# Kernel tuning notes

Measured on AMD Instinct MI355X. Metric: run time of the kernel, lower is better.

## Reference

```python
import jax, jax.numpy as jnp
import numpy as np

B, T, C = 4, 2048, 1024
N_HEAD = 16
HEAD_DIM = C // N_HEAD


def setup_inputs() -> dict:
    key = jax.random.key(0)
    k1, k2, k3 = jax.random.split(key, 3)
    x = jax.random.normal(k1, (B, T, C), dtype=jnp.float32)
    # Linear weights stored as (in, out); scaled like typical init
    w_qkv = jax.random.normal(k2, (C, 3 * C), dtype=jnp.float32) * (1.0 / np.sqrt(C))
    w_proj = jax.random.normal(k3, (C, C), dtype=jnp.float32) * (1.0 / np.sqrt(C))
    return {"x": x, "w_qkv": w_qkv, "w_proj": w_proj}


def reference(x, w_qkv, w_proj):
    b, t, c = x.shape
    qkv = x @ w_qkv                      # (B,T,3C)
    q, k, v = jnp.split(qkv, 3, axis=-1)
    # (B,H,T,D)
    def to_heads(a):
        return a.reshape(b, t, N_HEAD, HEAD_DIM).transpose(0, 2, 1, 3)
    q, k, v = to_heads(q), to_heads(k), to_heads(v)
    scale = 1.0 / np.sqrt(HEAD_DIM).astype(np.float32)
    att = jnp.einsum('bhqd,bhkd->bhqk', q, k) * scale   # (B,H,T,T)
    causal = jnp.tril(jnp.ones((t, t), dtype=bool))
    att = jnp.where(causal[None, None, :, :], att, -jnp.inf)
    att = jax.nn.softmax(att, axis=-1)
    # dropout p=0.0 (eval) -> identity
    y = jnp.einsum('bhqk,bhkd->bhqd', att, v)            # (B,H,T,D)
    y = y.transpose(0, 2, 1, 3).reshape(b, t, c)
    return y @ w_proj
```

## Files before the change

kernel.cpp:

```cpp
#include <hip/hip_runtime.h>
#include <hip/hip_bf16.h>
#include <stdint.h>

#define Bsz 4
#define Tsz 2048
#define Csz 1024
#define Hn  16
#define Dh  64
#define BH  (Bsz*Hn)
#define Mrows (Bsz*Tsz)
#define N1  (3*Csz)

typedef short s16x8 __attribute__((ext_vector_type(8)));
typedef short s16x4 __attribute__((ext_vector_type(4)));
typedef float fx4   __attribute__((ext_vector_type(4)));

static __device__ __forceinline__ short f2bf(float x) {
  __hip_bfloat16 h = __float2bfloat16(x);
  return __builtin_bit_cast(short, h);
}

#define GLDS16(g, l) __builtin_amdgcn_global_load_lds( \
    (const __attribute__((address_space(1))) void*)(g), \
    (__attribute__((address_space(3))) void*)(l), 16, 0, 0)

__global__ void cvt_kernel(const float* __restrict__ in, short* __restrict__ out, int n4) {
  int i = blockIdx.x * blockDim.x + threadIdx.x;
  int stride = blockDim.x * gridDim.x;
  for (; i < n4; i += stride) {
    float4 v = ((const float4*)in)[i];
    s16x4 o;
    o.x = f2bf(v.x); o.y = f2bf(v.y); o.z = f2bf(v.z); o.w = f2bf(v.w);
    ((s16x4*)out)[i] = o;
  }
}

__global__ void transpose_cvt_kernel(const float* __restrict__ w, short* __restrict__ wt,
                                     int K, int N) {
  __shared__ float tile[32][33];
  int tc = threadIdx.x & 31;
  int tr = threadIdx.x >> 5;
  int n0 = blockIdx.x * 32;
  int k0 = blockIdx.y * 32;
#pragma unroll
  for (int p = 0; p < 4; p++) {
    int r = tr + p*8;
    tile[r][tc] = w[(size_t)(k0 + r) * N + (n0 + tc)];
  }
  __syncthreads();
#pragma unroll
  for (int p = 0; p < 4; p++) {
    int r = tr + p*8;
    wt[(size_t)(n0 + r) * K + (k0 + tc)] = f2bf(tile[tc][r]);
  }
}

__global__ __launch_bounds__(256) void gemm_bt_kernel(
    const short* __restrict__ A, const short* __restrict__ Bt,
    float* __restrict__ Cf,
    short* __restrict__ Qo, short* __restrict__ Ko, short* __restrict__ Vo,
    int Mdim, int Ndim, int Kdim, int mode)
{
  __shared__ __align__(16) short sA[128*64];
  __shared__ __align__(16) short sB[128*64];
  const int tid  = threadIdx.x;
  const int lane = tid & 63;
  const int lr   = lane & 15;
  const int lq   = lane >> 4;
  const int wv   = tid >> 6;
  const int sw   = lr & 7;
  const int nb   = Ndim >> 7;
  const int bm   = (int)blockIdx.x / nb;
  const int bn   = (int)blockIdx.x % nb;
  const int m_off = (wv & 1) << 6;
  const int n_off = (wv >> 1) << 6;

  const short* Ab = A  + (size_t)bm * 128 * Kdim;
  const short* Bb = Bt + (size_t)bn * 128 * Kdim;

  fx4 acc[4][4];
#pragma unroll
  for (int i = 0; i < 4; i++)
#pragma unroll
    for (int j = 0; j < 4; j++) acc[i][j] = (fx4){0.f, 0.f, 0.f, 0.f};

  int cr[4], cg[4];
#pragma unroll
  for (int i = 0; i < 4; i++) {
    int c = tid + 256*i;
    cr[i] = c >> 3;
    cg[i] = ((c & 7) ^ (cr[i] & 7)) * 8;
  }

  for (int k0 = 0; k0 < Kdim; k0 += 64) {
    __syncthreads();
#pragma unroll
    for (int i = 0; i < 4; i++) {
      GLDS16(Ab + (size_t)cr[i] * Kdim + k0 + cg[i], sA + (tid + 256*i) * 8);
      GLDS16(Bb + (size_t)cr[i] * Kdim + k0 + cg[i], sB + (tid + 256*i) * 8);
    }
    __syncthreads();
    s16x8 af[4][2], bf[4][2];
#pragma unroll
    for (int mt = 0; mt < 4; mt++)
#pragma unroll
      for (int kk = 0; kk < 2; kk++)
        af[mt][kk] = *(const s16x8*)(sA + (m_off + mt*16 + lr)*64 + ((kk*4 + lq) ^ sw)*8);
#pragma unroll
    for (int nt = 0; nt < 4; nt++)
#pragma unroll
      for (int kk = 0; kk < 2; kk++)
        bf[nt][kk] = *(const s16x8*)(sB + (n_off + nt*16 + lr)*64 + ((kk*4 + lq) ^ sw)*8);
#pragma unroll
    for (int kk = 0; kk < 2; kk++)
#pragma unroll
      for (int mt = 0; mt < 4; mt++)
#pragma unroll
        for (int nt = 0; nt < 4; nt++)
          acc[mt][nt] = __builtin_amdgcn_mfma_f32_16x16x32_bf16(af[mt][kk], bf[nt][kk], acc[mt][nt], 0, 0, 0);
  }

  const int gm0 = bm*128 + m_off;
  const int gn0 = bn*128 + n_off;
  if (mode == 0) {
#pragma unroll
    for (int mt = 0; mt < 4; mt++)
#pragma unroll
      for (int nt = 0; nt < 4; nt++) {
        int col = gn0 + nt*16 + lr;
#pragma unroll
        for (int r = 0; r < 4; r++) {
          int row = gm0 + mt*16 + lq*4 + r;
          Cf[(size_t)row * Ndim + col] = acc[mt][nt][r];
        }
      }
  } else {
#pragma unroll
    for (int mt = 0; mt < 4; mt++)
#pragma unroll
      for (int nt = 0; nt < 4; nt++) {
        int n   = gn0 + nt*16 + lr;
        int sec = n >> 10;
        int cc  = n & 1023;
        int hh  = cc >> 6;
        int dd  = cc & 63;
#pragma unroll
        for (int r = 0; r < 4; r++) {
          int m  = gm0 + mt*16 + lq*4 + r;
          int bb = m >> 11;
          int tt = m & 2047;
          int bh = bb * Hn + hh;
          short v = f2bf(acc[mt][nt][r]);
          if (sec == 0)      Qo[((size_t)bh * Tsz + tt) * Dh + dd] = v;
          else if (sec == 1) Ko[((size_t)bh * Tsz + tt) * Dh + dd] = v;
          else               Vo[((size_t)bh * Dh + dd) * Tsz + tt] = v;
        }
      }
  }
}

#define PPITCH 72

__global__ __launch_bounds__(256) void attn_kernel(
    const short* __restrict__ Qb, const short* __restrict__ Kb,
    const short* __restrict__ Vt, short* __restrict__ Y)
{
  __shared__ __align__(16) short sK[64*64];
  __shared__ __align__(16) short sV[64*64];
  __shared__ __align__(16) short pbuf[4][32*PPITCH];
  const int tid  = threadIdx.x;
  const int lane = tid & 63;
  const int wv   = tid >> 6;
  const int lr   = lane & 15;
  const int lq   = lane >> 4;
  const int sw   = lr & 7;
  const int bh   = blockIdx.x;
  const int qb   = 15 - (int)blockIdx.y;
  const int b    = bh >> 4;
  const int h    = bh & 15;
  const int q0   = qb*128 + wv*32;

  const short* Qp = Qb + (size_t)bh * Tsz * Dh;
  const short* Kp = Kb + (size_t)bh * Tsz * Dh;
  const short* Vp = Vt + (size_t)bh * Dh * Tsz;
  short* pb = pbuf[wv];

  const int c0 = tid,       r0 = c0 >> 3, g0 = (((c0 & 7) ^ (r0 & 7)) * 8);
  const int c1 = tid + 256, r1 = c1 >> 3, g1 = (((c1 & 7) ^ (r1 & 7)) * 8);

  s16x8 bq[2][2];
#pragma unroll
  for (int j = 0; j < 2; j++)
#pragma unroll
    for (int kk = 0; kk < 2; kk++)
      bq[j][kk] = *(const s16x8*)(Qp + (size_t)(q0 + 16*j + lr)*Dh + kk*32 + lq*8);

  fx4 o[2][4];
#pragma unroll
  for (int j = 0; j < 2; j++)
#pragma unroll
    for (int i = 0; i < 4; i++) o[j][i] = (fx4){0.f, 0.f, 0.f, 0.f};
  float li[2] = {0.f, 0.f};
  const float sc = 0.125f * 1.44269504f;

  const int ntiles = 2*qb + 2;
  for (int kt = 0; kt < ntiles; kt++) {
    const int kbase = kt*64;
    __syncthreads();
    GLDS16(Kp + (size_t)(kbase + r0)*Dh + g0, sK + c0*8);
    GLDS16(Kp + (size_t)(kbase + r1)*Dh + g1, sK + c1*8);
    GLDS16(Vp + (size_t)r0*Tsz + kbase + g0, sV + c0*8);
    GLDS16(Vp + (size_t)r1*Tsz + kbase + g1, sV + c1*8);
    __syncthreads();

    if (kbase <= q0 + 31) {
      const bool masked = (kbase + 63 > q0);

      fx4 s[2][4];
#pragma unroll
      for (int j = 0; j < 2; j++)
#pragma unroll
        for (int mt = 0; mt < 4; mt++) s[j][mt] = (fx4){0.f,0.f,0.f,0.f};
#pragma unroll
      for (int mt = 0; mt < 4; mt++)
#pragma unroll
        for (int kk = 0; kk < 2; kk++) {
          const s16x8 akf = *(const s16x8*)(sK + (mt*16 + lr)*64 + ((kk*4 + lq) ^ sw)*8);
          s[0][mt] = __builtin_amdgcn_mfma_f32_16x16x32_bf16(akf, bq[0][kk], s[0][mt], 0, 0, 0);
          s[1][mt] = __builtin_amdgcn_mfma_f32_16x16x32_bf16(akf, bq[1][kk], s[1][mt], 0, 0, 0);
        }

#pragma unroll
      for (int j = 0; j < 2; j++) {
        const int qg = q0 + 16*j + lr;
        float p[16];
#pragma unroll
        for (int mt = 0; mt < 4; mt++)
#pragma unroll
          for (int r = 0; r < 4; r++) {
            float v = s[j][mt][r];
            if (masked) {
              int jg = kbase + mt*16 + lq*4 + r;
              v = (jg <= qg) ? v : -1e30f;
            }
            p[mt*4 + r] = __builtin_amdgcn_exp2f(v * sc);
          }
        float s8[8];
#pragma unroll
        for (int i = 0; i < 8; i++) s8[i] = p[i] + p[i+8];
        float s4[4];
#pragma unroll
        for (int i = 0; i < 4; i++) s4[i] = s8[i] + s8[i+4];
        li[j] += (s4[0] + s4[2]) + (s4[1] + s4[3]);
#pragma unroll
        for (int mt = 0; mt < 4; mt++) {
          s16x4 pk;
          pk.x = f2bf(p[mt*4+0]); pk.y = f2bf(p[mt*4+1]);
          pk.z = f2bf(p[mt*4+2]); pk.w = f2bf(p[mt*4+3]);
          *(s16x4*)(pb + (16*j + lr)*PPITCH + mt*16 + lq*4) = pk;
        }
      }
      __asm__ __volatile__("" ::: "memory");
      s16x8 pf[2][2];
#pragma unroll
      for (int j = 0; j < 2; j++)
#pragma unroll
        for (int kk = 0; kk < 2; kk++)
          pf[j][kk] = *(const s16x8*)(pb + (16*j + lr)*PPITCH + kk*32 + lq*8);
      __asm__ __volatile__("" ::: "memory");

#pragma unroll
      for (int dt = 0; dt < 4; dt++)
#pragma unroll
        for (int kk = 0; kk < 2; kk++) {
          const s16x8 avf = *(const s16x8*)(sV + (dt*16 + lr)*64 + ((kk*4 + lq) ^ sw)*8);
          o[0][dt] = __builtin_amdgcn_mfma_f32_16x16x32_bf16(avf, pf[0][kk], o[0][dt], 0, 0, 0);
          o[1][dt] = __builtin_amdgcn_mfma_f32_16x16x32_bf16(avf, pf[1][kk], o[1][dt], 0, 0, 0);
        }
    }
  }

#pragma unroll
  for (int j = 0; j < 2; j++) {
    float l = li[j];
    l += __shfl_xor(l, 16);
    l += __shfl_xor(l, 32);
    float inv = 1.0f / l;
#pragma unroll
    for (int dt = 0; dt < 4; dt++) {
      s16x4 yk;
      yk.x = f2bf(o[j][dt][0]*inv); yk.y = f2bf(o[j][dt][1]*inv);
      yk.z = f2bf(o[j][dt][2]*inv); yk.w = f2bf(o[j][dt][3]*inv);
      *(s16x4*)(Y + ((size_t)b*Tsz + q0 + 16*j + lr)*Csz + h*Dh + dt*16 + lq*4) = yk;
    }
  }
}

extern "C" void kernel_launch(void* const* d_in, const int* in_sizes, int n_in,
                              void* d_out, int out_size, void* d_ws, size_t ws_size,
                              hipStream_t stream)
{
  const float* x  = (const float*)d_in[0];
  const float* wq = (const float*)d_in[1];
  const float* wp = (const float*)d_in[2];
  float* out = (float*)d_out;

  char* ws = (char*)d_ws;
  size_t off = 0;
  short* xb  = (short*)(ws + off); off += (size_t)Mrows*Csz*2;
  short* wqT = (short*)(ws + off); off += (size_t)N1*Csz*2;
  short* wpT = (short*)(ws + off); off += (size_t)Csz*Csz*2;
  short* Qb  = (short*)(ws + off); off += (size_t)BH*Tsz*Dh*2;
  short* Kb  = (short*)(ws + off); off += (size_t)BH*Tsz*Dh*2;
  short* Vt  = (short*)(ws + off); off += (size_t)BH*Dh*Tsz*2;
  short* Yb  = (short*)(ws + off); off += (size_t)Mrows*Csz*2;

  cvt_kernel<<<1024, 256, 0, stream>>>(x, xb, Mrows*Csz/4);
  transpose_cvt_kernel<<<dim3(N1/32, Csz/32), 256, 0, stream>>>(wq, wqT, Csz, N1);
  transpose_cvt_kernel<<<dim3(Csz/32, Csz/32), 256, 0, stream>>>(wp, wpT, Csz, Csz);
  gemm_bt_kernel<<<(Mrows/128)*(N1/128), 256, 0, stream>>>(
      xb, wqT, nullptr, Qb, Kb, Vt, Mrows, N1, Csz, 1);
  attn_kernel<<<dim3(BH, Tsz/128), 256, 0, stream>>>(Qb, Kb, Vt, Yb);
  gemm_bt_kernel<<<(Mrows/128)*(Csz/128), 256, 0, stream>>>(
      Yb, wpT, out, nullptr, nullptr, nullptr, Mrows, Csz, Csz, 0);
}
```

Measured before the change: 278.4 us.

## Double-buffer LDS in QKV GEMM and attention, vectorize transposed V store

```diff
diff --git a/kernel.cpp b/kernel.cpp
--- a/kernel.cpp
+++ b/kernel.cpp
@@ -55,20 +55,59 @@
   }
 }
 
+static __device__ __forceinline__ void gemm_stage(
+    const short* __restrict__ Ab, const short* __restrict__ Bb, int Kdim, int k0,
+    short* __restrict__ sA, short* __restrict__ sB, int tid)
+{
+#pragma unroll
+  for (int i = 0; i < 2; i++) {
+    int c  = tid + 256*i;
+    int mr = c >> 3;
+    int l  = (c & 7) ^ (mr & 7);
+    int row = mr*2 + (l >> 2);
+    int ko  = (l & 3) * 8;
+    GLDS16(Ab + (size_t)row * Kdim + k0 + ko, sA + c*8);
+    GLDS16(Bb + (size_t)row * Kdim + k0 + ko, sB + c*8);
+  }
+}
+
+static __device__ __forceinline__ void gemm_compute(
+    const short* __restrict__ sA, const short* __restrict__ sB,
+    int m_off, int n_off, int lr, int lq, fx4 acc[4][4])
+{
+  s16x8 af[4], bf[4];
+#pragma unroll
+  for (int mt = 0; mt < 4; mt++) {
+    int m = m_off + mt*16 + lr, mr = m >> 1;
+    int p = (((m & 1)*4 + lq)) ^ (mr & 7);
+    af[mt] = *(const s16x8*)(sA + mr*64 + p*8);
+  }
+#pragma unroll
+  for (int nt = 0; nt < 4; nt++) {
+    int n = n_off + nt*16 + lr, nr = n >> 1;
+    int p = (((n & 1)*4 + lq)) ^ (nr & 7);
+    bf[nt] = *(const s16x8*)(sB + nr*64 + p*8);
+  }
+#pragma unroll
+  for (int mt = 0; mt < 4; mt++)
+#pragma unroll
+    for (int nt = 0; nt < 4; nt++)
+      acc[mt][nt] = __builtin_amdgcn_mfma_f32_16x16x32_bf16(af[mt], bf[nt], acc[mt][nt], 0, 0, 0);
+}
+
 __global__ __launch_bounds__(256) void gemm_bt_kernel(
     const short* __restrict__ A, const short* __restrict__ Bt,
     float* __restrict__ Cf,
     short* __restrict__ Qo, short* __restrict__ Ko, short* __restrict__ Vo,
     int Mdim, int Ndim, int Kdim, int mode)
 {
-  __shared__ __align__(16) short sA[128*64];
-  __shared__ __align__(16) short sB[128*64];
+  __shared__ __align__(16) short sA[2][128*32];
+  __shared__ __align__(16) short sB[2][128*32];
   const int tid  = threadIdx.x;
   const int lane = tid & 63;
   const int lr   = lane & 15;
   const int lq   = lane >> 4;
   const int wv   = tid >> 6;
-  const int sw   = lr & 7;
   const int nb   = Ndim >> 7;
   const int bm   = (int)blockIdx.x / nb;
   const int bn   = (int)blockIdx.x % nb;
@@ -84,40 +123,15 @@
 #pragma unroll
     for (int j = 0; j < 4; j++) acc[i][j] = (fx4){0.f, 0.f, 0.f, 0.f};
 
-  int cr[4], cg[4];
-#pragma unroll
-  for (int i = 0; i < 4; i++) {
-    int c = tid + 256*i;
-    cr[i] = c >> 3;
-    cg[i] = ((c & 7) ^ (cr[i] & 7)) * 8;
-  }
-
-  for (int k0 = 0; k0 < Kdim; k0 += 64) {
+  const int NIT = Kdim >> 5;
+  gemm_stage(Ab, Bb, Kdim, 0, sA[0], sB[0], tid);
+  for (int it = 0; it < NIT; it += 2) {
     __syncthreads();
-#pragma unroll
-    for (int i = 0; i < 4; i++) {
-      GLDS16(Ab + (size_t)cr[i] * Kdim + k0 + cg[i], sA + (tid + 256*i) * 8);
-      GLDS16(Bb + (size_t)cr[i] * Kdim + k0 + cg[i], sB + (tid + 256*i) * 8);
-    }
+    if (it + 1 < NIT) gemm_stage(Ab, Bb, Kdim, (it+1)*32, sA[1], sB[1], tid);
+    gemm_compute(sA[0], sB[0], m_off, n_off, lr, lq, acc);
     __syncthreads();
-    s16x8 af[4][2], bf[4][2];
-#pragma unroll
-    for (int mt = 0; mt < 4; mt++)
-#pragma unroll
-      for (int kk = 0; kk < 2; kk++)
-        af[mt][kk] = *(const s16x8*)(sA + (m_off + mt*16 + lr)*64 + ((kk*4 + lq) ^ sw)*8);
-#pragma unroll
-    for (int nt = 0; nt < 4; nt++)
-#pragma unroll
-      for (int kk = 0; kk < 2; kk++)
-        bf[nt][kk] = *(const s16x8*)(sB + (n_off + nt*16 + lr)*64 + ((kk*4 + lq) ^ sw)*8);
-#pragma unroll
-    for (int kk = 0; kk < 2; kk++)
-#pragma unroll
-      for (int mt = 0; mt < 4; mt++)
-#pragma unroll
-        for (int nt = 0; nt < 4; nt++)
-          acc[mt][nt] = __builtin_amdgcn_mfma_f32_16x16x32_bf16(af[mt][kk], bf[nt][kk], acc[mt][nt], 0, 0, 0);
+    if (it + 2 < NIT) gemm_stage(Ab, Bb, Kdim, (it+2)*32, sA[0], sB[0], tid);
+    gemm_compute(sA[1], sB[1], m_off, n_off, lr, lq, acc);
   }
 
   const int gm0 = bm*128 + m_off;
@@ -144,29 +158,120 @@
         int cc  = n & 1023;
         int hh  = cc >> 6;
         int dd  = cc & 63;
-#pragma unroll
-        for (int r = 0; r < 4; r++) {
-          int m  = gm0 + mt*16 + lq*4 + r;
-          int bb = m >> 11;
-          int tt = m & 2047;
-          int bh = bb * Hn + hh;
-          short v = f2bf(acc[mt][nt][r]);
-          if (sec == 0)      Qo[((size_t)bh * Tsz + tt) * Dh + dd] = v;
-          else if (sec == 1) Ko[((size_t)bh * Tsz + tt) * Dh + dd] = v;
-          else               Vo[((size_t)bh * Dh + dd) * Tsz + tt] = v;
+        if (sec == 2) {
+          int tt0 = gm0 + mt*16 + lq*4;
+          int bb  = tt0 >> 11;
+          int bh  = bb * Hn + hh;
+          s16x4 pk;
+          pk.x = f2bf(acc[mt][nt][0]); pk.y = f2bf(acc[mt][nt][1]);
+          pk.z = f2bf(acc[mt][nt][2]); pk.w = f2bf(acc[mt][nt][3]);
+          *(s16x4*)(Vo + ((size_t)bh * Dh + dd) * Tsz + (tt0 & 2047)) = pk;
+        } else {
+#pragma unroll
+          for (int r = 0; r < 4; r++) {
+            int m  = gm0 + mt*16 + lq*4 + r;
+            int bb = m >> 11;
+            int tt = m & 2047;
+            int bh = bb * Hn + hh;
+            short v = f2bf(acc[mt][nt][r]);
+            if (sec == 0) Qo[((size_t)bh * Tsz + tt) * Dh + dd] = v;
+            else          Ko[((size_t)bh * Tsz + tt) * Dh + dd] = v;
+          }
         }
       }
   }
 }
 
 #define PPITCH 72
+
+static __device__ __forceinline__ void attn_stage(
+    const short* __restrict__ Kp, const short* __restrict__ Vp, int kbase,
+    short* __restrict__ sK, short* __restrict__ sV,
+    int c0, int r0, int g0, int c1, int r1, int g1)
+{
+  GLDS16(Kp + (size_t)(kbase + r0)*Dh + g0, sK + c0*8);
+  GLDS16(Kp + (size_t)(kbase + r1)*Dh + g1, sK + c1*8);
+  GLDS16(Vp + (size_t)r0*Tsz + kbase + g0, sV + c0*8);
+  GLDS16(Vp + (size_t)r1*Tsz + kbase + g1, sV + c1*8);
+}
+
+static __device__ __forceinline__ void attn_compute(
+    const short* __restrict__ sK, const short* __restrict__ sV,
+    int kbase, int q0, int lr, int lq, int sw,
+    short* __restrict__ pb, const s16x8 bq[2][2], fx4 o[2][4], float li[2])
+{
+  const float sc = 0.125f * 1.44269504f;
+  const bool masked = (kbase + 63 > q0);
+
+  fx4 s[2][4];
+#pragma unroll
+  for (int j = 0; j < 2; j++)
+#pragma unroll
+    for (int mt = 0; mt < 4; mt++) s[j][mt] = (fx4){0.f,0.f,0.f,0.f};
+#pragma unroll
+  for (int mt = 0; mt < 4; mt++)
+#pragma unroll
+    for (int kk = 0; kk < 2; kk++) {
+      const s16x8 akf = *(const s16x8*)(sK + (mt*16 + lr)*64 + ((kk*4 + lq) ^ sw)*8);
+      s[0][mt] = __builtin_amdgcn_mfma_f32_16x16x32_bf16(akf, bq[0][kk], s[0][mt], 0, 0, 0);
+      s[1][mt] = __builtin_amdgcn_mfma_f32_16x16x32_bf16(akf, bq[1][kk], s[1][mt], 0, 0, 0);
+    }
+
+#pragma unroll
+  for (int j = 0; j < 2; j++) {
+    const int qg = q0 + 16*j + lr;
+    float p[16];
+#pragma unroll
+    for (int mt = 0; mt < 4; mt++)
+#pragma unroll
+      for (int r = 0; r < 4; r++) {
+        float v = s[j][mt][r];
+        if (masked) {
+          int jg = kbase + mt*16 + lq*4 + r;
+          v = (jg <= qg) ? v : -1e30f;
+        }
+        p[mt*4 + r] = __builtin_amdgcn_exp2f(v * sc);
+      }
+    float s8[8];
+#pragma unroll
+    for (int i = 0; i < 8; i++) s8[i] = p[i] + p[i+8];
+    float s4[4];
+#pragma unroll
+    for (int i = 0; i < 4; i++) s4[i] = s8[i] + s8[i+4];
+    li[j] += (s4[0] + s4[2]) + (s4[1] + s4[3]);
+#pragma unroll
+    for (int mt = 0; mt < 4; mt++) {
+      s16x4 pk;
+      pk.x = f2bf(p[mt*4+0]); pk.y = f2bf(p[mt*4+1]);
+      pk.z = f2bf(p[mt*4+2]); pk.w = f2bf(p[mt*4+3]);
+      *(s16x4*)(pb + (16*j + lr)*PPITCH + mt*16 + lq*4) = pk;
+    }
+  }
+  __asm__ __volatile__("" ::: "memory");
+  s16x8 pf[2][2];
+#pragma unroll
+  for (int j = 0; j < 2; j++)
+#pragma unroll
+    for (int kk = 0; kk < 2; kk++)
+      pf[j][kk] = *(const s16x8*)(pb + (16*j + lr)*PPITCH + kk*32 + lq*8);
+  __asm__ __volatile__("" ::: "memory");
+
+#pragma unroll
+  for (int dt = 0; dt < 4; dt++)
+#pragma unroll
+    for (int kk = 0; kk < 2; kk++) {
+      const s16x8 avf = *(const s16x8*)(sV + (dt*16 + lr)*64 + ((kk*4 + lq) ^ sw)*8);
+      o[0][dt] = __builtin_amdgcn_mfma_f32_16x16x32_bf16(avf, pf[0][kk], o[0][dt], 0, 0, 0);
+      o[1][dt] = __builtin_amdgcn_mfma_f32_16x16x32_bf16(avf, pf[1][kk], o[1][dt], 0, 0, 0);
+    }
+}
 
 __global__ __launch_bounds__(256) void attn_kernel(
     const short* __restrict__ Qb, const short* __restrict__ Kb,
     const short* __restrict__ Vt, short* __restrict__ Y)
 {
-  __shared__ __align__(16) short sK[64*64];
-  __shared__ __align__(16) short sV[64*64];
+  __shared__ __align__(16) short sK[2][64*64];
+  __shared__ __align__(16) short sV[2][64*64];
   __shared__ __align__(16) short pbuf[4][32*PPITCH];
   const int tid  = threadIdx.x;
   const int lane = tid & 63;
@@ -201,83 +306,18 @@
 #pragma unroll
     for (int i = 0; i < 4; i++) o[j][i] = (fx4){0.f, 0.f, 0.f, 0.f};
   float li[2] = {0.f, 0.f};
-  const float sc = 0.125f * 1.44269504f;
 
   const int ntiles = 2*qb + 2;
-  for (int kt = 0; kt < ntiles; kt++) {
-    const int kbase = kt*64;
+  attn_stage(Kp, Vp, 0, sK[0], sV[0], c0, r0, g0, c1, r1, g1);
+  for (int kt = 0; kt < ntiles; kt += 2) {
     __syncthreads();
-    GLDS16(Kp + (size_t)(kbase + r0)*Dh + g0, sK + c0*8);
-    GLDS16(Kp + (size_t)(kbase + r1)*Dh + g1, sK + c1*8);
-    GLDS16(Vp + (size_t)r0*Tsz + kbase + g0, sV + c0*8);
-    GLDS16(Vp + (size_t)r1*Tsz + kbase + g1, sV + c1*8);
+    if (kt + 1 < ntiles) attn_stage(Kp, Vp, (kt+1)*64, sK[1], sV[1], c0, r0, g0, c1, r1, g1);
+    if (kt*64 <= q0 + 31)
+      attn_compute(sK[0], sV[0], kt*64, q0, lr, lq, sw, pb, bq, o, li);
     __syncthreads();
-
-    if (kbase <= q0 + 31) {
-      const bool masked = (kbase + 63 > q0);
-
-      fx4 s[2][4];
-#pragma unroll
-      for (int j = 0; j < 2; j++)
-#pragma unroll
-        for (int mt = 0; mt < 4; mt++) s[j][mt] = (fx4){0.f,0.f,0.f,0.f};
-#pragma unroll
-      for (int mt = 0; mt < 4; mt++)
-#pragma unroll
-        for (int kk = 0; kk < 2; kk++) {
-          const s16x8 akf = *(const s16x8*)(sK + (mt*16 + lr)*64 + ((kk*4 + lq) ^ sw)*8);
-          s[0][mt] = __builtin_amdgcn_mfma_f32_16x16x32_bf16(akf, bq[0][kk], s[0][mt], 0, 0, 0);
-          s[1][mt] = __builtin_amdgcn_mfma_f32_16x16x32_bf16(akf, bq[1][kk], s[1][mt], 0, 0, 0);
-        }
-
-#pragma unroll
-      for (int j = 0; j < 2; j++) {
-        const int qg = q0 + 16*j + lr;
-        float p[16];
-#pragma unroll
-        for (int mt = 0; mt < 4; mt++)
-#pragma unroll
-          for (int r = 0; r < 4; r++) {
-            float v = s[j][mt][r];
-            if (masked) {
-              int jg = kbase + mt*16 + lq*4 + r;
-              v = (jg <= qg) ? v : -1e30f;
-            }
-            p[mt*4 + r] = __builtin_amdgcn_exp2f(v * sc);
-          }
-        float s8[8];
-#pragma unroll
-        for (int i = 0; i < 8; i++) s8[i] = p[i] + p[i+8];
-        float s4[4];
-#pragma unroll
-        for (int i = 0; i < 4; i++) s4[i] = s8[i] + s8[i+4];
-        li[j] += (s4[0] + s4[2]) + (s4[1] + s4[3]);
-#pragma unroll
-        for (int mt = 0; mt < 4; mt++) {
-          s16x4 pk;
-          pk.x = f2bf(p[mt*4+0]); pk.y = f2bf(p[mt*4+1]);
-          pk.z = f2bf(p[mt*4+2]); pk.w = f2bf(p[mt*4+3]);
-          *(s16x4*)(pb + (16*j + lr)*PPITCH + mt*16 + lq*4) = pk;
-        }
-      }
-      __asm__ __volatile__("" ::: "memory");
-      s16x8 pf[2][2];
-#pragma unroll
-      for (int j = 0; j < 2; j++)
-#pragma unroll
-        for (int kk = 0; kk < 2; kk++)
-          pf[j][kk] = *(const s16x8*)(pb + (16*j + lr)*PPITCH + kk*32 + lq*8);
-      __asm__ __volatile__("" ::: "memory");
-
-#pragma unroll
-      for (int dt = 0; dt < 4; dt++)
-#pragma unroll
-        for (int kk = 0; kk < 2; kk++) {
-          const s16x8 avf = *(const s16x8*)(sV + (dt*16 + lr)*64 + ((kk*4 + lq) ^ sw)*8);
-          o[0][dt] = __builtin_amdgcn_mfma_f32_16x16x32_bf16(avf, pf[0][kk], o[0][dt], 0, 0, 0);
-          o[1][dt] = __builtin_amdgcn_mfma_f32_16x16x32_bf16(avf, pf[1][kk], o[1][dt], 0, 0, 0);
-        }
-    }
+    if (kt + 2 < ntiles) attn_stage(Kp, Vp, (kt+2)*64, sK[0], sV[0], c0, r0, g0, c1, r1, g1);
+    if ((kt+1)*64 <= q0 + 31)
+      attn_compute(sK[1], sV[1], (kt+1)*64, q0, lr, lq, sw, pb, bq, o, li);
   }
 
 #pragma unroll
```

New measurement: 263.2 us. -5.4%, faster.
